# Kernel tuning notes

Measured on AMD Instinct MI355X. Metric: run time of the kernel, lower is better.

Reference implementation:

```python
import jax, jax.numpy as jnp
import numpy as np

IN_SZ = 256
OUT_SZ = 256
N_CHAN = 1024
RANK = 4  # min(4, IN_SZ*OUT_SZ)
B = 256
N = 2048


def setup_inputs() -> dict:
    key = jax.random.key(0)
    k_x, k_idx, k_u, k_v, k_b = jax.random.split(key, 5)
    x = jax.random.normal(k_x, (B, N, IN_SZ), dtype=jnp.float32)
    indices = jax.random.randint(k_idx, (B,), 0, N_CHAN)
    # init per reset_parameters(const=1.0)
    bound_u = np.sqrt(3.0 / RANK)              # fan_out of weights_U [C, r] is r
    weights_U = jax.random.uniform(k_u, (N_CHAN, RANK), jnp.float32, -bound_u, bound_u)
    bound_v = np.sqrt(1.0 / (IN_SZ * OUT_SZ))  # fan_out of weights_V [r, in*out]
    weights_V = jax.random.uniform(k_v, (RANK, IN_SZ * OUT_SZ), jnp.float32, -bound_v, bound_v)
    bound_b = np.sqrt(1.0 / RANK)
    bias = jax.random.uniform(k_b, (N_CHAN, 1, OUT_SZ), jnp.float32, -bound_b, bound_b)
    return {"x": x, "indices": indices, "weights_U": weights_U,
            "weights_V": weights_V, "bias": bias}


def reference(x, indices, weights_U, weights_V, bias):
    # weight synthesis: gather U rows first, then low-rank expand (same math as
    # full (U@V)[indices], without materializing unused channels)
    w = (weights_U[indices] @ weights_V).reshape(-1, IN_SZ, OUT_SZ)  # [B, in, out]
    out = jnp.einsum('bni,bio->bno', x, w)                            # [B, N, out]
    out = out + bias[indices]                                         # [B,1,out] broadcast
    return out
```

## Files before the change

kernel.cpp:

```cpp
#include <hip/hip_runtime.h>
#include <cstdint>

#define AS1 __attribute__((address_space(1)))
#define AS3 __attribute__((address_space(3)))

typedef __attribute__((ext_vector_type(8))) short short8;
typedef __attribute__((ext_vector_type(4))) float f32x4;

constexpr int SEQ   = 2048;
constexpr int INSZ  = 256;
constexpr int OUTSZ = 256;

__device__ __forceinline__ ushort f2bf(float f) {
  union { float f; uint32_t u; } v; v.f = f;
  uint32_t u = v.u;
  return (ushort)((u + 0x7FFFu + ((u >> 16) & 1u)) >> 16);
}
__device__ __forceinline__ uint32_t pk2(float a, float b) {
  return (uint32_t)f2bf(a) | ((uint32_t)f2bf(b) << 16);
}

__global__ __launch_bounds__(256) void synth_w(
    const float* __restrict__ U, const float* __restrict__ V,
    const int* __restrict__ idx, ushort* __restrict__ wsW)
{
  const int b   = blockIdx.y;
  const int kb  = blockIdx.x;
  const int tid = threadIdx.x;
  const int ch  = idx[b];
  const float u0 = U[ch*4+0], u1 = U[ch*4+1], u2 = U[ch*4+2], u3 = U[ch*4+3];

  __shared__ ushort tile[64][260];

  const int o4    = (tid & 63) * 4;
  const int kbase = (tid >> 6) * 16;
  for (int kk = 0; kk < 16; ++kk) {
    const int k  = kbase + kk;
    const int gk = kb*64 + k;
    const float* vp = V + (size_t)gk*OUTSZ + o4;
    float4 a = *(const float4*)(vp);
    float4 c = *(const float4*)(vp + 65536);
    float4 d = *(const float4*)(vp + 131072);
    float4 e = *(const float4*)(vp + 196608);
    ushort4 pkv;
    pkv.x = f2bf(u0*a.x + u1*c.x + u2*d.x + u3*e.x);
    pkv.y = f2bf(u0*a.y + u1*c.y + u2*d.y + u3*e.y);
    pkv.z = f2bf(u0*a.z + u1*c.z + u2*d.z + u3*e.z);
    pkv.w = f2bf(u0*a.w + u1*c.w + u2*d.w + u3*e.w);
    *(ushort4*)(&tile[k][o4]) = pkv;
  }
  __syncthreads();

  for (int s = 0; s < 8; ++s) {
    const int item = s*256 + tid;
    const int o    = item >> 3;
    const int cd   = item & 7;
    const int ks   = cd ^ (o & 7);
    uint4 pkv;
    pkv.x = (uint32_t)tile[ks*8+0][o] | ((uint32_t)tile[ks*8+1][o] << 16);
    pkv.y = (uint32_t)tile[ks*8+2][o] | ((uint32_t)tile[ks*8+3][o] << 16);
    pkv.z = (uint32_t)tile[ks*8+4][o] | ((uint32_t)tile[ks*8+5][o] << 16);
    pkv.w = (uint32_t)tile[ks*8+6][o] | ((uint32_t)tile[ks*8+7][o] << 16);
    uint4* dst = (uint4*)(wsW + (((size_t)(b*4 + kb))*256 + o)*64 + cd*8);
    *dst = pkv;
  }
}

__global__ __launch_bounds__(256) void lr_gemm(
    const float* __restrict__ x, const int* __restrict__ idx,
    const float* __restrict__ bias, const ushort* __restrict__ wsW,
    float* __restrict__ out)
{
  __shared__ ushort ldsA[64*64];
  __shared__ ushort ldsB[256*64];

  const int wg  = blockIdx.x;
  const int swz = (wg & 7) * 1024 + (wg >> 3);
  const int b     = swz >> 5;
  const int ntile = swz & 31;
  const int n0    = ntile * 64;

  const int tid  = threadIdx.x;
  const int lane = tid & 63;
  const int wave = tid >> 6;
  const int hi16 = lane >> 4;
  const int lo16 = lane & 15;

  const float*  xb = x   + ((size_t)b*SEQ + n0)*INSZ;
  const ushort* wb = wsW + (size_t)b*(4*256*64);

  f32x4 acc[4][4] = {};

  for (int kb = 0; kb < 4; ++kb) {
    for (int t = 0; t < 8; ++t) {
      const int chunk = wave*8 + t;
      const ushort* src = wb + kb*16384 + chunk*512 + lane*8;
      ushort* dstp = ldsB + chunk*512;
      __builtin_amdgcn_global_load_lds((const AS1 void*)src, (AS3 void*)dstp, 16, 0, 0);
    }
    for (int s = 0; s < 2; ++s) {
      const int item = s*256 + tid;
      const int row  = item >> 3;
      const int cs   = item & 7;
      const float* src = xb + (size_t)row*INSZ + kb*64 + cs*8;
      float4 f0 = *(const float4*)(src);
      float4 f1 = *(const float4*)(src + 4);
      uint4 pkv;
      pkv.x = pk2(f0.x, f0.y); pkv.y = pk2(f0.z, f0.w);
      pkv.z = pk2(f1.x, f1.y); pkv.w = pk2(f1.z, f1.w);
      const int cdd = cs ^ (row & 7);
      *(uint4*)(ldsA + row*64 + cdd*8) = pkv;
    }
    __syncthreads();

    for (int ks = 0; ks < 2; ++ks) {
      const int kbyte = ks*64 + hi16*16;
      short8 af[4], bfr[4];
      for (int m = 0; m < 4; ++m) {
        const int row = m*16 + lo16;
        af[m] = *(const short8*)((const char*)ldsA + row*128 + (kbyte ^ ((row & 7) << 4)));
      }
      for (int n = 0; n < 4; ++n) {
        const int o = wave*64 + n*16 + lo16;
        bfr[n] = *(const short8*)((const char*)ldsB + o*128 + (kbyte ^ ((o & 7) << 4)));
      }
      for (int m = 0; m < 4; ++m)
        for (int n = 0; n < 4; ++n)
          acc[m][n] = __builtin_amdgcn_mfma_f32_16x16x32_bf16(af[m], bfr[n], acc[m][n], 0, 0, 0);
    }
    __syncthreads();
  }

  const int ch = idx[b];
  const float* bb = bias + (size_t)ch*OUTSZ;
  float bv[4];
  for (int n = 0; n < 4; ++n) bv[n] = bb[wave*64 + n*16 + lo16];

  float* outb = out + ((size_t)b*SEQ + n0)*OUTSZ;
  for (int m = 0; m < 4; ++m) {
    const int rbase = m*16 + hi16*4;
    for (int n = 0; n < 4; ++n) {
      const int col = wave*64 + n*16 + lo16;
      #pragma unroll
      for (int j = 0; j < 4; ++j) {
        outb[(size_t)(rbase + j)*OUTSZ + col] = acc[m][n][j] + bv[n];
      }
    }
  }
}

extern "C" void kernel_launch(void* const* d_in, const int* in_sizes, int n_in,
                              void* d_out, int out_size, void* d_ws, size_t ws_size,
                              hipStream_t stream) {
  const float* x    = (const float*)d_in[0];
  const int*   idx  = (const int*)d_in[1];
  const float* U    = (const float*)d_in[2];
  const float* V    = (const float*)d_in[3];
  const float* bias = (const float*)d_in[4];
  float* out  = (float*)d_out;
  ushort* wsW = (ushort*)d_ws;

  synth_w<<<dim3(4, 256), 256, 0, stream>>>(U, V, idx, wsW);
  lr_gemm<<<8192, 256, 0, stream>>>(x, idx, bias, wsW, out);
}
```

Before: 257.6 us.

## Pre-swizzle weights into MFMA fragment order and load B directly from global

The weight-synthesis kernel now writes bf16 weights laid out exactly as per-lane MFMA B fragments, so the GEMM kernel reads them straight from global/L2 into registers instead of staging them through LDS. The whole 64x256 x tile is converted to bf16 into LDS once up front, which removes the per-k-block syncthreads and the B staging. Launch bounds request 4 blocks per CU to raise occupancy. This trades LDS traffic and barriers for more global/L2 fragment loads, which may stall the MFMAs if latency is not hidden.

```diff
diff --git a/kernel.cpp b/kernel.cpp
--- a/kernel.cpp
+++ b/kernel.cpp
@@ -1,8 +1,5 @@
 #include <hip/hip_runtime.h>
 #include <cstdint>
-
-#define AS1 __attribute__((address_space(1)))
-#define AS3 __attribute__((address_space(3)))
 
 typedef __attribute__((ext_vector_type(8))) short short8;
 typedef __attribute__((ext_vector_type(4))) float f32x4;
@@ -52,33 +49,34 @@
   __syncthreads();
 
   for (int s = 0; s < 8; ++s) {
-    const int item = s*256 + tid;
-    const int o    = item >> 3;
-    const int cd   = item & 7;
-    const int ks   = cd ^ (o & 7);
+    const int c      = s*256 + tid;
+    const int kshalf = c >> 10;
+    const int nb     = (c >> 6) & 15;
+    const int lane   = c & 63;
+    const int o      = nb*16 + (lane & 15);
+    const int k0     = kshalf*32 + (lane >> 4)*8;
     uint4 pkv;
-    pkv.x = (uint32_t)tile[ks*8+0][o] | ((uint32_t)tile[ks*8+1][o] << 16);
-    pkv.y = (uint32_t)tile[ks*8+2][o] | ((uint32_t)tile[ks*8+3][o] << 16);
-    pkv.z = (uint32_t)tile[ks*8+4][o] | ((uint32_t)tile[ks*8+5][o] << 16);
-    pkv.w = (uint32_t)tile[ks*8+6][o] | ((uint32_t)tile[ks*8+7][o] << 16);
-    uint4* dst = (uint4*)(wsW + (((size_t)(b*4 + kb))*256 + o)*64 + cd*8);
+    pkv.x = (uint32_t)tile[k0+0][o] | ((uint32_t)tile[k0+1][o] << 16);
+    pkv.y = (uint32_t)tile[k0+2][o] | ((uint32_t)tile[k0+3][o] << 16);
+    pkv.z = (uint32_t)tile[k0+4][o] | ((uint32_t)tile[k0+5][o] << 16);
+    pkv.w = (uint32_t)tile[k0+6][o] | ((uint32_t)tile[k0+7][o] << 16);
+    uint4* dst = (uint4*)(wsW + (size_t)b*65536 + (size_t)(2*kb + kshalf)*8192
+                              + nb*512 + lane*8);
     *dst = pkv;
   }
 }
 
-__global__ __launch_bounds__(256) void lr_gemm(
+__global__ __launch_bounds__(256, 4) void lr_gemm(
     const float* __restrict__ x, const int* __restrict__ idx,
     const float* __restrict__ bias, const ushort* __restrict__ wsW,
     float* __restrict__ out)
 {
-  __shared__ ushort ldsA[64*64];
-  __shared__ ushort ldsB[256*64];
+  __shared__ ushort ldsA[64*256];
 
   const int wg  = blockIdx.x;
   const int swz = (wg & 7) * 1024 + (wg >> 3);
   const int b     = swz >> 5;
-  const int ntile = swz & 31;
-  const int n0    = ntile * 64;
+  const int n0    = (swz & 31) * 64;
 
   const int tid  = threadIdx.x;
   const int lane = tid & 63;
@@ -86,59 +84,54 @@
   const int hi16 = lane >> 4;
   const int lo16 = lane & 15;
 
-  const float*  xb = x   + ((size_t)b*SEQ + n0)*INSZ;
-  const ushort* wb = wsW + (size_t)b*(4*256*64);
+  const float* xb = x + ((size_t)b*SEQ + n0)*INSZ;
+
+  #pragma unroll
+  for (int it = 0; it < 8; ++it) {
+    const int row = it*8 + (tid >> 5);
+    const int c8  = tid & 31;
+    const float* src = xb + (size_t)row*INSZ + c8*8;
+    float4 f0 = *(const float4*)(src);
+    float4 f1 = *(const float4*)(src + 4);
+    uint4 pkv;
+    pkv.x = pk2(f0.x, f0.y); pkv.y = pk2(f0.z, f0.w);
+    pkv.z = pk2(f1.x, f1.y); pkv.w = pk2(f1.z, f1.w);
+    *(uint4*)((char*)ldsA + row*512 + ((c8*16) ^ ((row & 7) << 4))) = pkv;
+  }
+  __syncthreads();
 
   f32x4 acc[4][4] = {};
+  const int sx = (lo16 & 7) << 4;
+  const ushort* wbp = wsW + (size_t)b*65536 + (size_t)(wave*4)*512 + lane*8;
+  const char*   aB  = (const char*)ldsA + lo16*512;
 
-  for (int kb = 0; kb < 4; ++kb) {
-    for (int t = 0; t < 8; ++t) {
-      const int chunk = wave*8 + t;
-      const ushort* src = wb + kb*16384 + chunk*512 + lane*8;
-      ushort* dstp = ldsB + chunk*512;
-      __builtin_amdgcn_global_load_lds((const AS1 void*)src, (AS3 void*)dstp, 16, 0, 0);
-    }
-    for (int s = 0; s < 2; ++s) {
-      const int item = s*256 + tid;
-      const int row  = item >> 3;
-      const int cs   = item & 7;
-      const float* src = xb + (size_t)row*INSZ + kb*64 + cs*8;
-      float4 f0 = *(const float4*)(src);
-      float4 f1 = *(const float4*)(src + 4);
-      uint4 pkv;
-      pkv.x = pk2(f0.x, f0.y); pkv.y = pk2(f0.z, f0.w);
-      pkv.z = pk2(f1.x, f1.y); pkv.w = pk2(f1.z, f1.w);
-      const int cdd = cs ^ (row & 7);
-      *(uint4*)(ldsA + row*64 + cdd*8) = pkv;
-    }
-    __syncthreads();
-
-    for (int ks = 0; ks < 2; ++ks) {
-      const int kbyte = ks*64 + hi16*16;
-      short8 af[4], bfr[4];
-      for (int m = 0; m < 4; ++m) {
-        const int row = m*16 + lo16;
-        af[m] = *(const short8*)((const char*)ldsA + row*128 + (kbyte ^ ((row & 7) << 4)));
-      }
-      for (int n = 0; n < 4; ++n) {
-        const int o = wave*64 + n*16 + lo16;
-        bfr[n] = *(const short8*)((const char*)ldsB + o*128 + (kbyte ^ ((o & 7) << 4)));
-      }
-      for (int m = 0; m < 4; ++m)
-        for (int n = 0; n < 4; ++n)
-          acc[m][n] = __builtin_amdgcn_mfma_f32_16x16x32_bf16(af[m], bfr[n], acc[m][n], 0, 0, 0);
-    }
-    __syncthreads();
+  #pragma unroll
+  for (int k5 = 0; k5 < 8; ++k5) {
+    short8 bf[4], af[4];
+    #pragma unroll
+    for (int n = 0; n < 4; ++n)
+      bf[n] = *(const short8*)(wbp + k5*8192 + n*512);
+    #pragma unroll
+    for (int m = 0; m < 4; ++m)
+      af[m] = *(const short8*)(aB + m*8192 + ((k5*64 + hi16*16) ^ sx));
+    #pragma unroll
+    for (int m = 0; m < 4; ++m)
+      #pragma unroll
+      for (int n = 0; n < 4; ++n)
+        acc[m][n] = __builtin_amdgcn_mfma_f32_16x16x32_bf16(af[m], bf[n], acc[m][n], 0, 0, 0);
   }
 
   const int ch = idx[b];
   const float* bb = bias + (size_t)ch*OUTSZ;
   float bv[4];
+  #pragma unroll
   for (int n = 0; n < 4; ++n) bv[n] = bb[wave*64 + n*16 + lo16];
 
   float* outb = out + ((size_t)b*SEQ + n0)*OUTSZ;
+  #pragma unroll
   for (int m = 0; m < 4; ++m) {
     const int rbase = m*16 + hi16*4;
+    #pragma unroll
     for (int n = 0; n < 4; ++n) {
       const int col = wave*64 + n*16 + lo16;
       #pragma unroll
```

Result: no change. 254.3 us (-1.3%).
